# Performance work log

Measured on AMD Instinct MI355X. Metric: run time of the kernel, lower is better.

The kernel has to match this reference:

```python
import jax, jax.numpy as jnp
import numpy as np

EPS = 1e-12


def l2_normalize(x, axis=-1, eps=EPS):
    return x * jax.lax.rsqrt((x * x).sum(axis=axis, keepdims=True) + eps)


def setup_inputs() -> dict:
    key = jax.random.key(0)
    k1, k2 = jax.random.split(key)
    B, S, E_DIM = 32, 1024, 32   # batch, tokens per image, codebook embed dim
    N_EMBED = 8192               # codebook size
    hidden_states = jax.random.normal(k1, (B, S, E_DIM), dtype=jnp.float32)
    # variance_scaling(1.0, 'fan_in', 'normal') over fan_in=E_DIM -> std = 1/sqrt(E_DIM)
    embedding = jax.random.normal(k2, (N_EMBED, E_DIM), dtype=jnp.float32) / jnp.sqrt(jnp.float32(E_DIM))
    return {"hidden_states": hidden_states, "embedding": embedding}


def reference(hidden_states, embedding):
    e_dim = embedding.shape[-1]
    # flatten to (N, e_dim) and L2-normalize both codes and inputs
    flat = l2_normalize(hidden_states.reshape(-1, e_dim), axis=1)   # (N, e_dim)
    emb = l2_normalize(embedding, axis=1)                           # (K, e_dim)
    # pairwise squared L2 distance: ||z||^2 + ||e||^2 - 2 z.e  -> (N, K)
    distance = (
        jnp.sum(flat * flat, axis=1, keepdims=True)
        + jnp.sum(emb * emb, axis=1)
        - 2.0 * jnp.dot(flat, emb.T)
    )
    min_encoding_indices = jnp.argmin(distance, axis=1).reshape(hidden_states.shape[0], -1)  # (B, S)
    # codebook lookup (gather raw embedding then renormalize, as in get_codebook_entry)
    z_q = l2_normalize(jnp.take(embedding, min_encoding_indices, axis=0), axis=-1)  # (B, S, e_dim)
    hidden_states_normed = l2_normalize(hidden_states, axis=-1)
    e_latent_loss = jnp.mean(jnp.square(jax.lax.stop_gradient(z_q) - hidden_states_normed))
    q_latent_loss = jnp.mean(jnp.square(z_q - jax.lax.stop_gradient(hidden_states_normed)))
    # straight-through estimator
    z_q = hidden_states + jax.lax.stop_gradient(z_q - hidden_states)
    return (z_q, min_encoding_indices, q_latent_loss, e_latent_loss)
```

## Files before the change

kernel.cpp:

```cpp
#include <hip/hip_runtime.h>
#include <math.h>

#define N_TOK   32768
#define K_CODES 8192
#define E_DIM   32
#define BLK     256
#define NCHUNK  4
#define TPC     128
#define TT      2
#define TAU     1.3e-4f
#define RG      2

#define OUT_IDX  1048576
#define OUT_QL   1081344
#define OUT_EL   1081345
#define OUTS_WMASK 655360
#define OUTS_BCNT  720896
#define OUTS_RZ    786432
#define OUTS_NSQ   802816

#define WSB_BPK    0
#define WSB_PBEST  1052672
#define WSB_PSEC   2101248
#define WSB_PIDX   3149824
#define WSB_FIDX   3674112
#define WSB_LPART  3805184

typedef __attribute__((ext_vector_type(8))) short bf16x8;
typedef __attribute__((ext_vector_type(4))) float f32x4;
typedef __attribute__((ext_vector_type(4))) double f64x4;

__device__ inline unsigned short bf16_rne(float x) {
  unsigned u = __builtin_bit_cast(unsigned, x);
  unsigned r = u + 0x7FFFu + ((u >> 16) & 1u);
  return (unsigned short)(r >> 16);
}
__device__ inline float bf16_to_f32(unsigned short h) {
  return __builtin_bit_cast(float, (unsigned)h << 16);
}

__global__ __launch_bounds__(BLK) void prep_kernel(
    const float* __restrict__ emb, char* __restrict__ Bpk,
    double* __restrict__ rza, double* __restrict__ nsqa)
{
  const int c = blockIdx.x * BLK + threadIdx.x;
  float z[E_DIM];
  const float4* p = (const float4*)(emb + c * E_DIM);
  float s = 0.f;
#pragma unroll
  for (int q = 0; q < 8; ++q) {
    float4 v = p[q];
    ((float4*)z)[q] = v;
    s += v.x * v.x + v.y * v.y + v.z * v.z + v.w * v.w;
  }
  const float rn = 1.f / sqrtf(s + 1e-12f);
  const int tile = c >> 4, row = c & 15;
#pragma unroll
  for (int g = 0; g < 4; ++g) {
    bf16x8 h8, l8;
#pragma unroll
    for (int j = 0; j < 8; ++j) {
      const float zn = z[g * 8 + j] * rn;
      const unsigned short h = bf16_rne(zn);
      h8[j] = (short)h;
      l8[j] = (short)bf16_rne(zn - bf16_to_f32(h));
    }
    char* base = Bpk + (size_t)tile * 2048 + (size_t)(g * 16 + row) * 16;
    *(bf16x8*)(base) = h8;
    *(bf16x8*)(base + 1024) = l8;
  }
  double n2 = 0.0;
#pragma unroll
  for (int j = 0; j < E_DIM; ++j) {
    const double e = (double)z[j];
    n2 = fma(e, e, n2);
  }
  const double rz = 1.0 / sqrt(n2 + 1e-12);
  double nsq = 0.0;
#pragma unroll
  for (int j = 0; j < E_DIM; ++j) {
    const double e = (double)z[j] * rz;
    nsq = fma(e, e, nsq);
  }
  rza[c] = rz;
  nsqa[c] = nsq;
}

__global__ __launch_bounds__(BLK) void screen_kernel(
    const float* __restrict__ hs, const char* __restrict__ Bpk,
    float* __restrict__ pbest, float* __restrict__ psec,
    unsigned short* __restrict__ pidx)
{
  const int lane = threadIdx.x & 63;
  const int wave = threadIdx.x >> 6;
  const int grp = lane >> 4, row = lane & 15;
  const int chunk = blockIdx.x >> 8;
  const int tb = blockIdx.x & 255;
  const int tile0 = tb * 8 + wave * TT;

  bf16x8 ahi[TT], alo[TT];
#pragma unroll
  for (int tt = 0; tt < TT; ++tt) {
    const float* ap = hs + ((tile0 + tt) * 16 + row) * E_DIM + grp * 8;
    float a[8];
    ((float4*)a)[0] = ((const float4*)ap)[0];
    ((float4*)a)[1] = ((const float4*)ap)[1];
    float ps = 0.f;
#pragma unroll
    for (int j = 0; j < 8; ++j) ps = fmaf(a[j], a[j], ps);
    ps += __shfl_xor(ps, 16, 64);
    ps += __shfl_xor(ps, 32, 64);
    const float rn = 1.f / sqrtf(ps + 1e-12f);
#pragma unroll
    for (int j = 0; j < 8; ++j) {
      const float zn = a[j] * rn;
      const unsigned short h = bf16_rne(zn);
      ahi[tt][j] = (short)h;
      alo[tt][j] = (short)bf16_rne(zn - bf16_to_f32(h));
    }
  }

  float best[TT][4], sec[TT][4];
  int bct[TT][4];
#pragma unroll
  for (int tt = 0; tt < TT; ++tt)
#pragma unroll
    for (int r = 0; r < 4; ++r) { best[tt][r] = -3e38f; sec[tt][r] = -3e38f; bct[tt][r] = 0; }

  const f32x4 Z4 = {0.f, 0.f, 0.f, 0.f};
  const char* Bc = Bpk + (size_t)(chunk * TPC) * 2048 + (size_t)lane * 16;

  bf16x8 h0 = *(const bf16x8*)(Bc);
  bf16x8 l0 = *(const bf16x8*)(Bc + 1024);
  for (int ct = 0; ct < TPC; ++ct) {
    const bf16x8 ch = h0, cl = l0;
    const char* pn = Bc + (size_t)(ct + 1) * 2048;
    h0 = *(const bf16x8*)(pn);
    l0 = *(const bf16x8*)(pn + 1024);
    f32x4 acc[TT];
#pragma unroll
    for (int tt = 0; tt < TT; ++tt) {
      acc[tt] = __builtin_amdgcn_mfma_f32_16x16x32_bf16(ahi[tt], ch, Z4, 0, 0, 0);
      acc[tt] = __builtin_amdgcn_mfma_f32_16x16x32_bf16(ahi[tt], cl, acc[tt], 0, 0, 0);
      acc[tt] = __builtin_amdgcn_mfma_f32_16x16x32_bf16(alo[tt], ch, acc[tt], 0, 0, 0);
    }
#pragma unroll
    for (int tt = 0; tt < TT; ++tt)
#pragma unroll
      for (int r = 0; r < 4; ++r) {
        const float d = acc[tt][r];
        sec[tt][r] = __builtin_amdgcn_fmed3f(best[tt][r], sec[tt][r], d);
        if (d > best[tt][r]) { best[tt][r] = d; bct[tt][r] = ct; }
      }
  }

  const int base = chunk * N_TOK;
#pragma unroll
  for (int tt = 0; tt < TT; ++tt) {
#pragma unroll
    for (int r = 0; r < 4; ++r) {
      float b = best[tt][r], s = sec[tt][r];
      int id = bct[tt][r] * 16 + row;
#pragma unroll
      for (int w = 1; w < 16; w <<= 1) {
        const float ob = __shfl_xor(b, w, 64);
        const float os = __shfl_xor(s, w, 64);
        const int   oi = __shfl_xor(id, w, 64);
        s = fmaxf(fmaxf(s, os), fminf(b, ob));
        if (ob > b || (ob == b && oi < id)) id = oi;
        b = fmaxf(b, ob);
      }
      if (row == 0) {
        const int tok = (tile0 + tt) * 16 + grp * 4 + r;
        pbest[base + tok] = b;
        psec[base + tok] = s;
        pidx[base + tok] = (unsigned short)(chunk * 2048 + id);
      }
    }
  }
}

__global__ __launch_bounds__(BLK) void merge_kernel(
    const float* __restrict__ pbest, const float* __restrict__ psec,
    const unsigned short* __restrict__ pidx, int* __restrict__ fidx,
    unsigned long long* __restrict__ wmask, int* __restrict__ bcount)
{
  const int t = blockIdx.x * BLK + threadIdx.x;
  float best = -3e38f, sec = -3e38f;
  int code = 0;
#pragma unroll
  for (int ch = 0; ch < NCHUNK; ++ch) {
    const float b = pbest[ch * N_TOK + t];
    const float s = psec[ch * N_TOK + t];
    const int c = pidx[ch * N_TOK + t];
    if (b > best) { sec = fmaxf(best, s); best = b; code = c; }
    else          { sec = fmaxf(sec, b); }
  }
  fidx[t] = code;
  const bool f = (best - sec < TAU);
  __shared__ int wcnt[4];
  const unsigned long long m = __ballot(f);
  const int lane = threadIdx.x & 63, wv = threadIdx.x >> 6;
  if (lane == 0) {
    wmask[blockIdx.x * 4 + wv] = m;
    wcnt[wv] = (int)__popcll(m);
  }
  __syncthreads();
  if (threadIdx.x == 0)
    bcount[blockIdx.x] = wcnt[0] + wcnt[1] + wcnt[2] + wcnt[3];
}

__global__ __launch_bounds__(256, 1) void recheck_kernel(
    const float* __restrict__ hs, const float* __restrict__ emb,
    const double* __restrict__ rza, const double* __restrict__ nsqa,
    const int* __restrict__ bcount, const unsigned long long* __restrict__ wmask,
    int* __restrict__ fidx)
{
  __shared__ int pfx[128], bcs[128], ssh[RG];
  __shared__ __align__(16) double zsh[RG][E_DIM];
  __shared__ int tsh[RG];
  __shared__ double rvW[RG][4];
  __shared__ int riW[RG][4];
  const int tid = threadIdx.x;
  const int lane = tid & 63, wv = tid >> 6;

  if (tid < 128) { const int c = bcount[tid]; bcs[tid] = c; pfx[tid] = c; }
  __syncthreads();
#pragma unroll
  for (int off = 1; off < 128; off <<= 1) {
    int v = 0;
    if (tid >= off && tid < 128) v = pfx[tid - off];
    __syncthreads();
    if (tid < 128) pfx[tid] += v;
    __syncthreads();
  }
  const int nflag = pfx[127];

  for (int base = blockIdx.x * RG; base < nflag; base += gridDim.x * RG) {
    __syncthreads();
    if (tid < 128) {
#pragma unroll
      for (int g = 0; g < RG; ++g) {
        const int rank = base + g;
        if (rank < nflag) {
          const bool gt = pfx[tid] > rank;
          const bool ple = (tid == 0) ? true : (pfx[tid - 1] <= rank);
          if (gt && ple) ssh[g] = tid;
        }
      }
    }
    __syncthreads();
    if (tid < RG) {
      const int rank = base + tid;
      int t = -1;
      if (rank < nflag) {
        const int s = ssh[tid];
        int r = rank - (pfx[s] - bcs[s]);
        int word = 0;
        unsigned long long w = wmask[s * 4];
        int c = (int)__popcll(w);
        while (r >= c) { r -= c; ++word; w = wmask[s * 4 + word]; c = (int)__popcll(w); }
#pragma unroll
        for (int half = 32; half > 0; half >>= 1) {
          const unsigned long long lm = (1ull << half) - 1ull;
          const int cc = (int)__popcll(w & lm);
          if (r >= cc) { r -= cc; w >>= half; t += 0; }
          if (r + cc >= 0) {}
          if (r >= 0 && false) {}
          if ((int)__popcll(0ull)) {}
        }
        r = rank - (pfx[s] - bcs[s]);
        word = 0;
        w = wmask[s * 4];
        c = (int)__popcll(w);
        while (r >= c) { r -= c; ++word; w = wmask[s * 4 + word]; c = (int)__popcll(w); }
        int pos = 0;
#pragma unroll
        for (int half = 32; half > 0; half >>= 1) {
          const unsigned long long lm = (half == 32) ? 0xFFFFFFFFull : ((1ull << half) - 1ull);
          const int cc = (int)__popcll(w & lm);
          if (r >= cc) { r -= cc; w >>= half; pos += half; }
        }
        t = s * 256 + word * 64 + pos;
      }
      tsh[tid] = t;
    }
    __syncthreads();
    if (tid < 32 * RG) {
      const int g = tid >> 5, j = tid & 31;
      const int t = tsh[g];
      const double zj = (t >= 0) ? (double)hs[t * E_DIM + j] : 0.0;
      double sq = zj * zj;
#pragma unroll
      for (int o = 16; o > 0; o >>= 1) sq += __shfl_xor(sq, o, 32);
      const double rzt = 1.0 / sqrt(sq + 1e-12);
      zsh[g][j] = zj * rzt;
    }
    __syncthreads();

    double bobj[RG];
    int bidx[RG];
#pragma unroll
    for (int g = 0; g < RG; ++g) { bobj[g] = 1e300; bidx[g] = 0x7fffffff; }

    for (int c = tid; c < K_CODES; c += 256) {
      const float4* ep = (const float4*)(emb + c * E_DIM);
      f64x4 e64[8];
#pragma unroll
      for (int q = 0; q < 8; ++q) {
        const float4 v = ep[q];
        e64[q][0] = (double)v.x; e64[q][1] = (double)v.y;
        e64[q][2] = (double)v.z; e64[q][3] = (double)v.w;
      }
      const double rzc = rza[c], nsqc = nsqa[c];
#pragma unroll
      for (int g = 0; g < RG; ++g) {
        double d0 = 0.0, d1 = 0.0;
#pragma unroll
        for (int q = 0; q < 8; q += 2) {
#pragma unroll
          for (int x = 0; x < 4; ++x) {
            d0 = fma(e64[q][x],     zsh[g][q * 4 + x],       d0);
            d1 = fma(e64[q + 1][x], zsh[g][(q + 1) * 4 + x], d1);
          }
        }
        const double obj = fma(-2.0, (d0 + d1) * rzc, nsqc);
        if (obj < bobj[g]) { bobj[g] = obj; bidx[g] = c; }
      }
    }

#pragma unroll
    for (int g = 0; g < RG; ++g) {
      double b = bobj[g]; int i = bidx[g];
#pragma unroll
      for (int o = 32; o > 0; o >>= 1) {
        const double ob = __shfl_down(b, o, 64);
        const int oi = __shfl_down(i, o, 64);
        if (ob < b || (ob == b && oi < i)) { b = ob; i = oi; }
      }
      if (lane == 0) { rvW[g][wv] = b; riW[g][wv] = i; }
    }
    __syncthreads();
    if (tid < RG) {
      const int g = tid;
      double b = rvW[g][0]; int i = riW[g][0];
#pragma unroll
      for (int w = 1; w < 4; ++w) {
        const double ob = rvW[g][w]; const int oi = riW[g][w];
        if (ob < b || (ob == b && oi < i)) { b = ob; i = oi; }
      }
      const int t = tsh[g];
      if (t >= 0) fidx[t] = i;
    }
  }
}

__global__ __launch_bounds__(BLK) void finalize_kernel(
    const float* __restrict__ hs, const float* __restrict__ emb,
    const int* __restrict__ fidx, float* __restrict__ out,
    float* __restrict__ lpart)
{
  const int t = blockIdx.x * BLK + threadIdx.x;
  const int idx = fidx[t];
  const float4* ep = (const float4*)(emb + idx * E_DIM);
  const float4* hp = (const float4*)(hs + t * E_DIM);
  float4 e[8], h[8];
  float se = 0.f, sh = 0.f;
#pragma unroll
  for (int q = 0; q < 8; ++q) {
    e[q] = ep[q]; h[q] = hp[q];
    se += e[q].x * e[q].x + e[q].y * e[q].y + e[q].z * e[q].z + e[q].w * e[q].w;
    sh += h[q].x * h[q].x + h[q].y * h[q].y + h[q].z * h[q].z + h[q].w * h[q].w;
  }
  const float re = 1.f / sqrtf(se + 1e-12f);
  const float rh = 1.f / sqrtf(sh + 1e-12f);
  float4* zo = (float4*)(out + t * E_DIM);
  float err = 0.f;
#pragma unroll
  for (int q = 0; q < 8; ++q) {
    float4 zq, hn;
    zq.x = e[q].x * re; zq.y = e[q].y * re; zq.z = e[q].z * re; zq.w = e[q].w * re;
    hn.x = h[q].x * rh; hn.y = h[q].y * rh; hn.z = h[q].z * rh; hn.w = h[q].w * rh;
    float dx = zq.x - hn.x, dy = zq.y - hn.y, dz = zq.z - hn.z, dw = zq.w - hn.w;
    err += dx * dx + dy * dy + dz * dz + dw * dw;
    zo[q] = zq;
  }
  out[OUT_IDX + t] = (float)idx;
#pragma unroll
  for (int o = 32; o > 0; o >>= 1) err += __shfl_down(err, o);
  if ((threadIdx.x & 63) == 0) lpart[t >> 6] = err;
}

__global__ __launch_bounds__(256) void loss_kernel(
    const float* __restrict__ lpart, float* __restrict__ out)
{
  const int tid = threadIdx.x;
  float a = lpart[tid] + lpart[tid + 256];
#pragma unroll
  for (int o = 32; o > 0; o >>= 1) a += __shfl_down(a, o);
  __shared__ float w[4];
  if ((tid & 63) == 0) w[tid >> 6] = a;
  __syncthreads();
  if (tid == 0) {
    const float tot = (w[0] + w[1]) + (w[2] + w[3]);
    const float c = tot * (1.0f / 1048576.0f);
    out[OUT_QL] = c;
    out[OUT_EL] = c;
  }
}

extern "C" void kernel_launch(void* const* d_in, const int* in_sizes, int n_in,
                              void* d_out, int out_size, void* d_ws, size_t ws_size,
                              hipStream_t stream) {
  (void)in_sizes; (void)n_in; (void)out_size; (void)ws_size;
  const float* hs  = (const float*)d_in[0];
  const float* emb = (const float*)d_in[1];
  float* out = (float*)d_out;
  char* wsb = (char*)d_ws;

  char*           Bpk   = wsb + WSB_BPK;
  float*          pbest = (float*)(wsb + WSB_PBEST);
  float*          psec  = (float*)(wsb + WSB_PSEC);
  unsigned short* pidx  = (unsigned short*)(wsb + WSB_PIDX);
  int*            fidx  = (int*)(wsb + WSB_FIDX);
  float*          lpart = (float*)(wsb + WSB_LPART);
  unsigned long long* wmask = (unsigned long long*)(out + OUTS_WMASK);
  int*            bcount  = (int*)(out + OUTS_BCNT);
  double*         rza     = (double*)(out + OUTS_RZ);
  double*         nsqa    = (double*)(out + OUTS_NSQ);

  prep_kernel<<<dim3(K_CODES / BLK), BLK, 0, stream>>>(emb, Bpk, rza, nsqa);
  screen_kernel<<<dim3(NCHUNK * 256), BLK, 0, stream>>>(hs, Bpk, pbest, psec, pidx);
  merge_kernel<<<dim3(N_TOK / BLK), BLK, 0, stream>>>(pbest, psec, pidx, fidx, wmask, bcount);
  recheck_kernel<<<dim3(2048), 256, 0, stream>>>(hs, emb, rza, nsqa, bcount, wmask, fidx);
  finalize_kernel<<<dim3(N_TOK / BLK), BLK, 0, stream>>>(hs, emb, fidx, out, lpart);
  loss_kernel<<<dim3(1), 256, 0, stream>>>(lpart, out);
}
```

Measured before the change: 119.2 us.

## Fuse merge with finalize and let recheck patch outputs in place

New measurement: 117.9 us. No clear change (-1.0%).

```diff
diff --git a/kernel.cpp b/kernel.cpp
--- a/kernel.cpp
+++ b/kernel.cpp
@@ -14,17 +14,16 @@
 #define OUT_IDX  1048576
 #define OUT_QL   1081344
 #define OUT_EL   1081345
-#define OUTS_WMASK 655360
-#define OUTS_BCNT  720896
-#define OUTS_RZ    786432
-#define OUTS_NSQ   802816
 
 #define WSB_BPK    0
 #define WSB_PBEST  1052672
 #define WSB_PSEC   2101248
 #define WSB_PIDX   3149824
-#define WSB_FIDX   3674112
 #define WSB_LPART  3805184
+#define WSB_WMASK  3807232
+#define WSB_BCNT   3811328
+#define WSB_RZ     3815424
+#define WSB_NSQ    3880960
 
 typedef __attribute__((ext_vector_type(8))) short bf16x8;
 typedef __attribute__((ext_vector_type(4))) float f32x4;
@@ -180,10 +179,12 @@
   }
 }
 
-__global__ __launch_bounds__(BLK) void merge_kernel(
+__global__ __launch_bounds__(BLK) void merge_fin_kernel(
+    const float* __restrict__ hs, const float* __restrict__ emb,
     const float* __restrict__ pbest, const float* __restrict__ psec,
-    const unsigned short* __restrict__ pidx, int* __restrict__ fidx,
-    unsigned long long* __restrict__ wmask, int* __restrict__ bcount)
+    const unsigned short* __restrict__ pidx,
+    unsigned long long* __restrict__ wmask, int* __restrict__ bcount,
+    float* __restrict__ out, float* __restrict__ lpart)
 {
   const int t = blockIdx.x * BLK + threadIdx.x;
   float best = -3e38f, sec = -3e38f;
@@ -196,7 +197,6 @@
     if (b > best) { sec = fmaxf(best, s); best = b; code = c; }
     else          { sec = fmaxf(sec, b); }
   }
-  fidx[t] = code;
   const bool f = (best - sec < TAU);
   __shared__ int wcnt[4];
   const unsigned long long m = __ballot(f);
@@ -208,17 +208,45 @@
   __syncthreads();
   if (threadIdx.x == 0)
     bcount[blockIdx.x] = wcnt[0] + wcnt[1] + wcnt[2] + wcnt[3];
+
+  const float4* ep = (const float4*)(emb + code * E_DIM);
+  const float4* hp = (const float4*)(hs + t * E_DIM);
+  float4 e[8], h[8];
+  float se = 0.f, sh = 0.f;
+#pragma unroll
+  for (int q = 0; q < 8; ++q) {
+    e[q] = ep[q]; h[q] = hp[q];
+    se += e[q].x * e[q].x + e[q].y * e[q].y + e[q].z * e[q].z + e[q].w * e[q].w;
+    sh += h[q].x * h[q].x + h[q].y * h[q].y + h[q].z * h[q].z + h[q].w * h[q].w;
+  }
+  const float re = 1.f / sqrtf(se + 1e-12f);
+  const float rh = 1.f / sqrtf(sh + 1e-12f);
+  float4* zo = (float4*)(out + t * E_DIM);
+  float err = 0.f;
+#pragma unroll
+  for (int q = 0; q < 8; ++q) {
+    float4 zq, hn;
+    zq.x = e[q].x * re; zq.y = e[q].y * re; zq.z = e[q].z * re; zq.w = e[q].w * re;
+    hn.x = h[q].x * rh; hn.y = h[q].y * rh; hn.z = h[q].z * rh; hn.w = h[q].w * rh;
+    float dx = zq.x - hn.x, dy = zq.y - hn.y, dz = zq.z - hn.z, dw = zq.w - hn.w;
+    err += dx * dx + dy * dy + dz * dz + dw * dw;
+    zo[q] = zq;
+  }
+  out[OUT_IDX + t] = (float)code;
+#pragma unroll
+  for (int o = 32; o > 0; o >>= 1) err += __shfl_down(err, o);
+  if (lane == 0) lpart[t >> 6] = err;
 }
 
 __global__ __launch_bounds__(256, 1) void recheck_kernel(
     const float* __restrict__ hs, const float* __restrict__ emb,
     const double* __restrict__ rza, const double* __restrict__ nsqa,
     const int* __restrict__ bcount, const unsigned long long* __restrict__ wmask,
-    int* __restrict__ fidx)
+    float* __restrict__ out)
 {
   __shared__ int pfx[128], bcs[128], ssh[RG];
   __shared__ __align__(16) double zsh[RG][E_DIM];
-  __shared__ int tsh[RG];
+  __shared__ int tsh[RG], riF[RG];
   __shared__ double rvW[RG][4];
   __shared__ int riW[RG][4];
   const int tid = threadIdx.x;
@@ -260,20 +288,6 @@
         unsigned long long w = wmask[s * 4];
         int c = (int)__popcll(w);
         while (r >= c) { r -= c; ++word; w = wmask[s * 4 + word]; c = (int)__popcll(w); }
-#pragma unroll
-        for (int half = 32; half > 0; half >>= 1) {
-          const unsigned long long lm = (1ull << half) - 1ull;
-          const int cc = (int)__popcll(w & lm);
-          if (r >= cc) { r -= cc; w >>= half; t += 0; }
-          if (r + cc >= 0) {}
-          if (r >= 0 && false) {}
-          if ((int)__popcll(0ull)) {}
-        }
-        r = rank - (pfx[s] - bcs[s]);
-        word = 0;
-        w = wmask[s * 4];
-        c = (int)__popcll(w);
-        while (r >= c) { r -= c; ++word; w = wmask[s * 4 + word]; c = (int)__popcll(w); }
         int pos = 0;
 #pragma unroll
         for (int half = 32; half > 0; half >>= 1) {
@@ -349,46 +363,25 @@
         const double ob = rvW[g][w]; const int oi = riW[g][w];
         if (ob < b || (ob == b && oi < i)) { b = ob; i = oi; }
       }
+      riF[g] = i;
       const int t = tsh[g];
-      if (t >= 0) fidx[t] = i;
-    }
-  }
-}
-
-__global__ __launch_bounds__(BLK) void finalize_kernel(
-    const float* __restrict__ hs, const float* __restrict__ emb,
-    const int* __restrict__ fidx, float* __restrict__ out,
-    float* __restrict__ lpart)
-{
-  const int t = blockIdx.x * BLK + threadIdx.x;
-  const int idx = fidx[t];
-  const float4* ep = (const float4*)(emb + idx * E_DIM);
-  const float4* hp = (const float4*)(hs + t * E_DIM);
-  float4 e[8], h[8];
-  float se = 0.f, sh = 0.f;
-#pragma unroll
-  for (int q = 0; q < 8; ++q) {
-    e[q] = ep[q]; h[q] = hp[q];
-    se += e[q].x * e[q].x + e[q].y * e[q].y + e[q].z * e[q].z + e[q].w * e[q].w;
-    sh += h[q].x * h[q].x + h[q].y * h[q].y + h[q].z * h[q].z + h[q].w * h[q].w;
-  }
-  const float re = 1.f / sqrtf(se + 1e-12f);
-  const float rh = 1.f / sqrtf(sh + 1e-12f);
-  float4* zo = (float4*)(out + t * E_DIM);
-  float err = 0.f;
-#pragma unroll
-  for (int q = 0; q < 8; ++q) {
-    float4 zq, hn;
-    zq.x = e[q].x * re; zq.y = e[q].y * re; zq.z = e[q].z * re; zq.w = e[q].w * re;
-    hn.x = h[q].x * rh; hn.y = h[q].y * rh; hn.z = h[q].z * rh; hn.w = h[q].w * rh;
-    float dx = zq.x - hn.x, dy = zq.y - hn.y, dz = zq.z - hn.z, dw = zq.w - hn.w;
-    err += dx * dx + dy * dy + dz * dz + dw * dw;
-    zo[q] = zq;
-  }
-  out[OUT_IDX + t] = (float)idx;
-#pragma unroll
-  for (int o = 32; o > 0; o >>= 1) err += __shfl_down(err, o);
-  if ((threadIdx.x & 63) == 0) lpart[t >> 6] = err;
+      if (t >= 0) out[OUT_IDX + t] = (float)i;
+    }
+    __syncthreads();
+    if (tid < 32 * RG) {
+      const int g = tid >> 5, j = tid & 31;
+      const int t = tsh[g];
+      if (t >= 0) {
+        const int i = riF[g];
+        const float ev = emb[i * E_DIM + j];
+        float sq = ev * ev;
+#pragma unroll
+        for (int o = 16; o > 0; o >>= 1) sq += __shfl_xor(sq, o, 32);
+        const float re = 1.f / sqrtf(sq + 1e-12f);
+        out[t * E_DIM + j] = ev * re;
+      }
+    }
+  }
 }
 
 __global__ __launch_bounds__(256) void loss_kernel(
@@ -422,17 +415,16 @@
   float*          pbest = (float*)(wsb + WSB_PBEST);
   float*          psec  = (float*)(wsb + WSB_PSEC);
   unsigned short* pidx  = (unsigned short*)(wsb + WSB_PIDX);
-  int*            fidx  = (int*)(wsb + WSB_FIDX);
   float*          lpart = (float*)(wsb + WSB_LPART);
-  unsigned long long* wmask = (unsigned long long*)(out + OUTS_WMASK);
-  int*            bcount  = (int*)(out + OUTS_BCNT);
-  double*         rza     = (double*)(out + OUTS_RZ);
-  double*         nsqa    = (double*)(out + OUTS_NSQ);
+  unsigned long long* wmask = (unsigned long long*)(wsb + WSB_WMASK);
+  int*            bcount  = (int*)(wsb + WSB_BCNT);
+  double*         rza     = (double*)(wsb + WSB_RZ);
+  double*         nsqa    = (double*)(wsb + WSB_NSQ);
 
   prep_kernel<<<dim3(K_CODES / BLK), BLK, 0, stream>>>(emb, Bpk, rza, nsqa);
   screen_kernel<<<dim3(NCHUNK * 256), BLK, 0, stream>>>(hs, Bpk, pbest, psec, pidx);
-  merge_kernel<<<dim3(N_TOK / BLK), BLK, 0, stream>>>(pbest, psec, pidx, fidx, wmask, bcount);
-  recheck_kernel<<<dim3(2048), 256, 0, stream>>>(hs, emb, rza, nsqa, bcount, wmask, fidx);
-  finalize_kernel<<<dim3(N_TOK / BLK), BLK, 0, stream>>>(hs, emb, fidx, out, lpart);
+  merge_fin_kernel<<<dim3(N_TOK / BLK), BLK, 0, stream>>>(hs, emb, pbest, psec, pidx,
+                                                          wmask, bcount, out, lpart);
+  recheck_kernel<<<dim3(2048), 256, 0, stream>>>(hs, emb, rza, nsqa, bcount, wmask, out);
   loss_kernel<<<dim3(1), 256, 0, stream>>>(lpart, out);
 }
```
